# Kernel tuning notes

Hardware: AMD Instinct MI355X
Metric: run time of the kernel (lower is better)

Reference implementation:

```python
import jax, jax.numpy as jnp
import numpy as np

H = 16
D_MODEL = 1024
BLOCK_SIZE = 64
B, S = 2, 2048
NEG = -65504.0  # value used by the torch module for masking


def setup_inputs() -> dict:
    key = jax.random.key(0)
    ks = jax.random.split(key, 12)
    scale = 1.0 / np.sqrt(D_MODEL)
    inp = {
        "query": jax.random.normal(ks[0], (B, S, D_MODEL), jnp.float32),
        "key": jax.random.normal(ks[1], (B, S, D_MODEL), jnp.float32),
        "value": jax.random.normal(ks[2], (B, S, D_MODEL), jnp.float32),
        "Wq": jax.random.normal(ks[3], (D_MODEL, D_MODEL), jnp.float32) * scale,
        "bq": jnp.zeros((D_MODEL,), jnp.float32),
        "Wk": jax.random.normal(ks[4], (D_MODEL, D_MODEL), jnp.float32) * scale,
        "bk": jnp.zeros((D_MODEL,), jnp.float32),
        "Wv": jax.random.normal(ks[5], (D_MODEL, D_MODEL), jnp.float32) * scale,
        "bv": jnp.zeros((D_MODEL,), jnp.float32),
        "Wo": jax.random.normal(ks[6], (D_MODEL, D_MODEL), jnp.float32) * scale,
        "bo": jnp.zeros((D_MODEL,), jnp.float32),
    }
    return inp


def reference(query, key, value, Wq, bq, Wk, bk, Wv, bv, Wo, bo):
    b, s, d = query.shape
    dk = d // H

    def proj(x, W, bias):
        # [b,s,d] -> [b,h,s,dk]
        return (x @ W + bias).reshape(b, s, H, dk).transpose(0, 2, 1, 3)

    q = proj(query, Wq, bq)
    k = proj(key, Wk, bk)
    v = proj(value, Wv, bv)

    # dense QK^T / sqrt(d_k), exactly as the torch module (then block mask added)
    scores = jnp.einsum("bhqd,bhkd->bhqk", q, k) / jnp.sqrt(jnp.float32(dk))

    bid = jnp.arange(s) // BLOCK_SIZE
    attn_mask = jnp.where(bid[:, None] == bid[None, :], 0.0, NEG).astype(scores.dtype)
    scores = scores + attn_mask  # broadcast over [b,h]

    attn = jax.nn.softmax(scores, axis=-1)
    x = jnp.einsum("bhqk,bhkd->bhqd", attn, v)
    x = x.transpose(0, 2, 1, 3).reshape(b, s, d)
    return x @ Wo + bo
```

## Files before the change

kernel.cpp:

```cpp
#include <hip/hip_runtime.h>
#include <hip/hip_bf16.h>

typedef __attribute__((ext_vector_type(4))) float f32x4;
typedef __attribute__((ext_vector_type(8))) short s16x8;

#define MFMA16(a, b, c) __builtin_amdgcn_mfma_f32_16x16x32_bf16(a, b, c, 0, 0, 0)

__device__ __forceinline__ void gld_lds16(const void* g, void* l) {
  __builtin_amdgcn_global_load_lds(
      (const __attribute__((address_space(1))) unsigned int*)g,
      (__attribute__((address_space(3))) unsigned int*)l, 16, 0, 0);
}

__device__ __forceinline__ unsigned short f2bf(float f) {
  union { __hip_bfloat16 b; unsigned short u; } cv;
  cv.b = __float2bfloat16(f);
  return cv.u;
}
__device__ __forceinline__ float bf2f(unsigned short u) {
  union { unsigned short u; __hip_bfloat16 b; } cv;
  cv.u = u;
  return __bfloat162float(cv.b);
}

__global__ void transw(const float* W0, unsigned short* H0,
                       const float* W1, unsigned short* H1,
                       const float* W2, unsigned short* H2,
                       const float* W3, unsigned short* H3) {
  __shared__ float tile[64 * 65];
  const float* W; unsigned short* H;
  switch (blockIdx.y) {
    case 0: W = W0; H = H0; break;
    case 1: W = W1; H = H1; break;
    case 2: W = W2; H = H2; break;
    default: W = W3; H = H3; break;
  }
  const int t = threadIdx.x;
  const int tk0 = (blockIdx.x & 15) * 64;
  const int tn0 = (blockIdx.x >> 4) * 64;
  for (int i = 0; i < 16; ++i) {
    int idx = i * 256 + t;
    int r = idx >> 6, c = idx & 63;
    tile[r * 65 + c] = W[(size_t)(tk0 + r) * 1024 + tn0 + c];
  }
  __syncthreads();
  for (int i = 0; i < 16; ++i) {
    int idx = i * 256 + t;
    int r = idx >> 6, c = idx & 63;
    H[(size_t)(tn0 + r) * 1024 + tk0 + c] = f2bf(tile[c * 65 + r]);
  }
}

__global__ void convert_x3(const float* A0, unsigned short* H0,
                           const float* A1, unsigned short* H1,
                           const float* A2, unsigned short* H2) {
  const float* src; unsigned short* h;
  switch (blockIdx.y) {
    case 0: src = A0; h = H0; break;
    case 1: src = A1; h = H1; break;
    default: src = A2; h = H2; break;
  }
  int i = blockIdx.x * 256 + threadIdx.x;
  float4 v = ((const float4*)src)[i];
  ((ushort4*)h)[i] = make_ushort4(f2bf(v.x), f2bf(v.y), f2bf(v.z), f2bf(v.w));
}

struct QkvArgs {
  const unsigned short* A[3];
  const unsigned short* B[3];
  const float* bias[3];
  unsigned short* out[3];
};

__global__ __launch_bounds__(512, 2)
void gemm_qkv(QkvArgs args) {
  const int K = 1024;
  __shared__ __align__(16) unsigned short lds[4][2][8192];
  const int tid = threadIdx.x;
  const int lane = tid & 63, w = tid >> 6;

  const int nwg = 192;
  const int orig = blockIdx.x;
  const int swz = (orig & 7) * (nwg >> 3) + (orig >> 3);
  const int g = swz >> 6;
  const int tl = swz & 63;
  const int m0 = (tl >> 2) * 256, n0 = (tl & 3) * 256;

  const unsigned short* A = args.A[g];
  const unsigned short* B = args.B[g];
  const float* bias = args.bias[g];
  unsigned short* out = args.out[g];

  const int wm = (w >> 2) * 128, wn = (w & 3) * 64;
  const int fr = lane & 15, gh = lane >> 4;

  size_t aoff[2], boff[2]; int dst[2];
  #pragma unroll
  for (int i = 0; i < 2; ++i) {
    const int G = i * 512 + tid;
    const int rp = G >> 3, spr = G & 7;
    const int s = spr ^ (rp & 7);
    const int srow = 2 * rp + (s >> 2), ko = (s & 3) * 8;
    aoff[i] = (size_t)(m0 + srow) * K + ko;
    boff[i] = (size_t)(n0 + srow) * K + ko;
    dst[i] = G * 8;
  }

  auto stage = [&](int buf, int kt) {
    #pragma unroll
    for (int i = 0; i < 2; ++i) {
      gld_lds16(A + aoff[i] + kt, &lds[buf][0][dst[i]]);
      gld_lds16(B + boff[i] + kt, &lds[buf][1][dst[i]]);
    }
  };

  f32x4 acc[8][4] = {};
  const int laneoff = (fr >> 1) * 64 + ((((fr & 1) << 2) | gh) ^ (fr >> 1)) * 8;

  stage(0, 0); stage(1, 32); stage(2, 64); stage(3, 96);

  #pragma unroll 1
  for (int t = 0; t < 32; ++t) {
    if (t < 29)      { asm volatile("s_waitcnt vmcnt(12)" ::: "memory"); }
    else if (t == 29){ asm volatile("s_waitcnt vmcnt(8)"  ::: "memory"); }
    else if (t == 30){ asm volatile("s_waitcnt vmcnt(4)"  ::: "memory"); }
    else             { asm volatile("s_waitcnt vmcnt(0)"  ::: "memory"); }
    __builtin_amdgcn_s_barrier();

    const int buf = t & 3;
    const unsigned short* La = &lds[buf][0][wm * 32 + laneoff];
    const unsigned short* Lb = &lds[buf][1][wn * 32 + laneoff];
    s16x8 b[4], a[8];
    #pragma unroll
    for (int nt = 0; nt < 4; ++nt) b[nt] = *(const s16x8*)&Lb[nt * 512];
    #pragma unroll
    for (int mt = 0; mt < 8; ++mt) a[mt] = *(const s16x8*)&La[mt * 512];
    #pragma unroll
    for (int mt = 0; mt < 8; ++mt)
      #pragma unroll
      for (int nt = 0; nt < 4; ++nt)
        acc[mt][nt] = MFMA16(a[mt], b[nt], acc[mt][nt]);

    __builtin_amdgcn_sched_barrier(0);
    __builtin_amdgcn_s_barrier();
    if (t + 4 < 32) stage(buf, (t + 4) * 32);
  }

  float bv[4];
  #pragma unroll
  for (int nt = 0; nt < 4; ++nt) bv[nt] = bias[n0 + wn + nt * 16 + fr];
  if (g == 2) {
    #pragma unroll
    for (int mt = 0; mt < 8; ++mt) {
      const int gm = m0 + wm + mt * 16 + (gh << 2);
      const int b = gm >> 11, s = gm & 2047;
      #pragma unroll
      for (int nt = 0; nt < 4; ++nt) {
        const int gn = n0 + wn + nt * 16 + fr;
        const int h = gn >> 6, d = gn & 63;
        f32x4 r = acc[mt][nt];
        ushort4 w4 = make_ushort4(f2bf(r[0] + bv[nt]), f2bf(r[1] + bv[nt]),
                                  f2bf(r[2] + bv[nt]), f2bf(r[3] + bv[nt]));
        *(ushort4*)&out[((size_t)((b * 16 + h) * 64 + d)) * 2048 + s] = w4;
      }
    }
  } else {
    #pragma unroll
    for (int mt = 0; mt < 8; ++mt) {
      const int gm = m0 + wm + mt * 16 + (gh << 2);
      #pragma unroll
      for (int nt = 0; nt < 4; ++nt) {
        const int gn = n0 + wn + nt * 16 + fr;
        f32x4 r = acc[mt][nt];
        #pragma unroll
        for (int j = 0; j < 4; ++j) {
          const int row = gm + j;
          size_t off = (((size_t)((row >> 11) * 16 + (gn >> 6))) * 2048 + (row & 2047)) * 64 + (gn & 63);
          out[off] = f2bf(r[j] + bv[nt]);
        }
      }
    }
  }
}

__global__ __launch_bounds__(256, 3)
void gemm_oproj(const unsigned short* __restrict__ A, const unsigned short* __restrict__ B,
                const float* __restrict__ bias, float* __restrict__ out) {
  const int K = 1024, N = 1024;
  __shared__ __align__(16) unsigned short lds[3][2][4096];
  const int tid = threadIdx.x;
  const int lane = tid & 63, wid = tid >> 6;

  const int nwg = 256;
  const int orig = blockIdx.x;
  const int swz = (orig & 7) * (nwg >> 3) + (orig >> 3);
  const int m0 = (swz >> 3) * 128, n0 = (swz & 7) * 128;

  const int wm = (wid >> 1) * 64, wn = (wid & 1) * 64;
  const int fr = lane & 15, gh = lane >> 4;

  size_t aoff[2], boff[2]; int dst[2];
  #pragma unroll
  for (int i = 0; i < 2; ++i) {
    const int G = i * 256 + tid;
    const int rp = G >> 3, spr = G & 7;
    const int s = spr ^ (rp & 7);
    const int srow = 2 * rp + (s >> 2), ko = (s & 3) * 8;
    aoff[i] = (size_t)(m0 + srow) * K + ko;
    boff[i] = (size_t)(n0 + srow) * K + ko;
    dst[i] = G * 8;
  }

  auto stage = [&](int buf, int kt) {
    #pragma unroll
    for (int i = 0; i < 2; ++i) {
      gld_lds16(A + aoff[i] + kt, &lds[buf][0][dst[i]]);
      gld_lds16(B + boff[i] + kt, &lds[buf][1][dst[i]]);
    }
  };

  f32x4 acc[4][4] = {};
  const int laneoff = (fr >> 1) * 64 + ((((fr & 1) << 2) | gh) ^ (fr >> 1)) * 8;

  stage(0, 0); stage(1, 32); stage(2, 64);

  #pragma unroll 1
  for (int t = 0; t < 32; ++t) {
    if (t < 30)      { asm volatile("s_waitcnt vmcnt(8)" ::: "memory"); }
    else if (t == 30){ asm volatile("s_waitcnt vmcnt(4)" ::: "memory"); }
    else             { asm volatile("s_waitcnt vmcnt(0)" ::: "memory"); }
    __builtin_amdgcn_s_barrier();

    const int buf = t % 3;
    const unsigned short* La = &lds[buf][0][wm * 32 + laneoff];
    const unsigned short* Lb = &lds[buf][1][wn * 32 + laneoff];
    s16x8 b[4], a[4];
    #pragma unroll
    for (int nt = 0; nt < 4; ++nt) b[nt] = *(const s16x8*)&Lb[nt * 512];
    #pragma unroll
    for (int mt = 0; mt < 4; ++mt) a[mt] = *(const s16x8*)&La[mt * 512];
    #pragma unroll
    for (int mt = 0; mt < 4; ++mt)
      #pragma unroll
      for (int nt = 0; nt < 4; ++nt)
        acc[mt][nt] = MFMA16(a[mt], b[nt], acc[mt][nt]);

    __builtin_amdgcn_sched_barrier(0);
    __builtin_amdgcn_s_barrier();
    if (t + 3 < 32) stage(buf, (t + 3) * 32);
  }

  #pragma unroll
  for (int mt = 0; mt < 4; ++mt) {
    const int gm = m0 + wm + mt * 16 + (gh << 2);
    #pragma unroll
    for (int nt = 0; nt < 4; ++nt) {
      const int gn = n0 + wn + nt * 16 + fr;
      const float bvv = bias[gn];
      f32x4 r = acc[mt][nt];
      #pragma unroll
      for (int j = 0; j < 4; ++j)
        out[(size_t)(gm + j) * N + gn] = r[j] + bvv;
    }
  }
}

__global__ __launch_bounds__(256, 2)
void attn_mfma(const unsigned short* __restrict__ Q, const unsigned short* __restrict__ Kb,
               const unsigned short* __restrict__ Vt, unsigned short* __restrict__ X) {
  __shared__ __align__(16) unsigned short qs[4096];
  __shared__ __align__(16) unsigned short ks2[4096];
  __shared__ __align__(16) unsigned short vs[4096];
  __shared__ __align__(16) unsigned short ps[4096];
  const int tid = threadIdx.x, lane = tid & 63, w = tid >> 6;
  const int hb = blockIdx.x >> 5, qb = blockIdx.x & 31;
  const size_t qkbase = ((size_t)hb * 2048 + qb * 64) * 64;
  const size_t vbase = (size_t)hb * 64 * 2048 + qb * 64;

  #pragma unroll
  for (int i = 0; i < 2; ++i) {
    const int G = i * 256 + tid;
    const int row = G >> 3, slot = G & 7;
    const int sg = slot ^ (row & 7);
    gld_lds16(Q + qkbase + row * 64 + sg * 8, &qs[G * 8]);
    gld_lds16(Kb + qkbase + row * 64 + sg * 8, &ks2[G * 8]);
    gld_lds16(Vt + vbase + (size_t)row * 2048 + sg * 8, &vs[G * 8]);
  }
  asm volatile("s_waitcnt vmcnt(0)" ::: "memory");
  __syncthreads();

  const int fr = lane & 15, gh = lane >> 4;
  const int arow = w * 16 + fr;

  s16x8 aq[2], bk[2][4];
  #pragma unroll
  for (int ks = 0; ks < 2; ++ks) {
    aq[ks] = *(const s16x8*)&qs[arow * 64 + (((ks * 4 + gh) ^ (arow & 7)) << 3)];
    #pragma unroll
    for (int nt = 0; nt < 4; ++nt) {
      const int krow = nt * 16 + fr;
      bk[ks][nt] = *(const s16x8*)&ks2[krow * 64 + (((ks * 4 + gh) ^ (krow & 7)) << 3)];
    }
  }
  f32x4 s[4] = {};
  #pragma unroll
  for (int ks = 0; ks < 2; ++ks)
    #pragma unroll
    for (int nt = 0; nt < 4; ++nt)
      s[nt] = MFMA16(aq[ks], bk[ks][nt], s[nt]);

  #pragma unroll
  for (int j = 0; j < 4; ++j) {
    float t0 = s[0][j] * 0.125f, t1 = s[1][j] * 0.125f;
    float t2 = s[2][j] * 0.125f, t3 = s[3][j] * 0.125f;
    float m = fmaxf(fmaxf(t0, t1), fmaxf(t2, t3));
    m = fmaxf(m, __shfl_xor(m, 1, 64));
    m = fmaxf(m, __shfl_xor(m, 2, 64));
    m = fmaxf(m, __shfl_xor(m, 4, 64));
    m = fmaxf(m, __shfl_xor(m, 8, 64));
    t0 = __expf(t0 - m); t1 = __expf(t1 - m);
    t2 = __expf(t2 - m); t3 = __expf(t3 - m);
    float sum = t0 + t1 + t2 + t3;
    sum += __shfl_xor(sum, 1, 64);
    sum += __shfl_xor(sum, 2, 64);
    sum += __shfl_xor(sum, 4, 64);
    sum += __shfl_xor(sum, 8, 64);
    const float r = 1.0f / sum;
    s[0][j] = t0 * r; s[1][j] = t1 * r; s[2][j] = t2 * r; s[3][j] = t3 * r;
  }

  #pragma unroll
  for (int j = 0; j < 4; ++j) {
    const int q = w * 16 + gh * 4 + j;
    #pragma unroll
    for (int nt = 0; nt < 4; ++nt) {
      const int k = nt * 16 + fr;
      ps[q * 64 + (((k >> 3) ^ (q & 7)) << 3) + (k & 7)] = f2bf(s[nt][j]);
    }
  }

  s16x8 ap[2], bv2[2][4];
  #pragma unroll
  for (int ks = 0; ks < 2; ++ks) {
    ap[ks] = *(const s16x8*)&ps[arow * 64 + (((ks * 4 + gh) ^ (arow & 7)) << 3)];
    #pragma unroll
    for (int nt = 0; nt < 4; ++nt) {
      const int drow = nt * 16 + fr;
      bv2[ks][nt] = *(const s16x8*)&vs[drow * 64 + (((ks * 4 + gh) ^ (drow & 7)) << 3)];
    }
  }
  f32x4 x[4] = {};
  #pragma unroll
  for (int ks = 0; ks < 2; ++ks)
    #pragma unroll
    for (int nt = 0; nt < 4; ++nt)
      x[nt] = MFMA16(ap[ks], bv2[ks][nt], x[nt]);

  const int b = hb >> 4, h = hb & 15;
  #pragma unroll
  for (int nt = 0; nt < 4; ++nt)
    #pragma unroll
    for (int j = 0; j < 4; ++j) {
      const int sgl = qb * 64 + w * 16 + gh * 4 + j;
      X[((size_t)(b * 2048 + sgl)) * 1024 + h * 64 + nt * 16 + fr] = f2bf(x[nt][j]);
    }
}

extern "C" void kernel_launch(void* const* d_in, const int* in_sizes, int n_in,
                              void* d_out, int out_size, void* d_ws, size_t ws_size,
                              hipStream_t stream) {
  const float* query = (const float*)d_in[0];
  const float* key   = (const float*)d_in[1];
  const float* value = (const float*)d_in[2];
  const float* Wq = (const float*)d_in[3]; const float* bq = (const float*)d_in[4];
  const float* Wk = (const float*)d_in[5]; const float* bk = (const float*)d_in[6];
  const float* Wv = (const float*)d_in[7]; const float* bv = (const float*)d_in[8];
  const float* Wo = (const float*)d_in[9]; const float* bo = (const float*)d_in[10];
  float* out = (float*)d_out;

  const size_t W_E = 1024 * 1024;
  const size_t X_E = 4096 * 1024;
  unsigned char* p = (unsigned char*)d_ws;
  auto take = [&](size_t bytes) { void* r = (void*)p; p += bytes; return r; };

  unsigned short* wtq = (unsigned short*)take(W_E * 2);
  unsigned short* wtk = (unsigned short*)take(W_E * 2);
  unsigned short* wtv = (unsigned short*)take(W_E * 2);
  unsigned short* wto = (unsigned short*)take(W_E * 2);
  unsigned short* xq = (unsigned short*)take(X_E * 2);
  unsigned short* xk = (unsigned short*)take(X_E * 2);
  unsigned short* xv = (unsigned short*)take(X_E * 2);
  unsigned short* Qb = (unsigned short*)take(X_E * 2);
  unsigned short* Kb = (unsigned short*)take(X_E * 2);
  unsigned short* Vt = (unsigned short*)take(X_E * 2);
  unsigned short* ao = (unsigned short*)take(X_E * 2);
  (void)ws_size; (void)in_sizes; (void)n_in; (void)out_size;

  transw<<<dim3(256, 4), 256, 0, stream>>>(Wq, wtq, Wk, wtk, Wv, wtv, Wo, wto);
  convert_x3<<<dim3(4096, 3), 256, 0, stream>>>(query, xq, key, xk, value, xv);

  QkvArgs qkv = {};
  qkv.A[0] = xq; qkv.B[0] = wtq; qkv.bias[0] = bq; qkv.out[0] = Qb;
  qkv.A[1] = xk; qkv.B[1] = wtk; qkv.bias[1] = bk; qkv.out[1] = Kb;
  qkv.A[2] = xv; qkv.B[2] = wtv; qkv.bias[2] = bv; qkv.out[2] = Vt;
  gemm_qkv<<<dim3(192), 512, 0, stream>>>(qkv);

  attn_mfma<<<dim3(1024), 256, 0, stream>>>(Qb, Kb, Vt, ao);

  gemm_oproj<<<dim3(256), 256, 0, stream>>>(ao, wto, bo, out);
}
```

Measured before the change: 86.72 us.

## Restructure GEMM main loops into ping-pong phases with interleaved loads and setprio

Both projection GEMM kernels now issue the next global-to-LDS stage inside the iteration, overlapped with the MFMA work, instead of after it. The QKV GEMM splits each k-step into two halves, loading A then B for a stage three steps ahead, with barriers between halves and s_setprio raised around the MFMA blocks. The output GEMM keeps a prefetch distance of two instead of three and moves its vmcnt wait to the end of the iteration. The intent is to hide LDS reads and global load issue behind matrix math and reduce stalls at barriers. In exchange there are more barriers per iteration, and the reuse of LDS buffers needs exact waitcnt bookkeeping to avoid races.

```diff
diff --git a/kernel.cpp b/kernel.cpp
--- a/kernel.cpp
+++ b/kernel.cpp
@@ -106,44 +106,68 @@
     dst[i] = G * 8;
   }
 
-  auto stage = [&](int buf, int kt) {
-    #pragma unroll
-    for (int i = 0; i < 2; ++i) {
-      gld_lds16(A + aoff[i] + kt, &lds[buf][0][dst[i]]);
-      gld_lds16(B + boff[i] + kt, &lds[buf][1][dst[i]]);
-    }
+  auto stageA = [&](int buf, int kt) {
+    gld_lds16(A + aoff[0] + kt, &lds[buf][0][dst[0]]);
+    gld_lds16(A + aoff[1] + kt, &lds[buf][0][dst[1]]);
+  };
+  auto stageB = [&](int buf, int kt) {
+    gld_lds16(B + boff[0] + kt, &lds[buf][1][dst[0]]);
+    gld_lds16(B + boff[1] + kt, &lds[buf][1][dst[1]]);
   };
 
   f32x4 acc[8][4] = {};
   const int laneoff = (fr >> 1) * 64 + ((((fr & 1) << 2) | gh) ^ (fr >> 1)) * 8;
 
-  stage(0, 0); stage(1, 32); stage(2, 64); stage(3, 96);
+  stageA(0, 0);  stageB(0, 0);
+  stageA(1, 32); stageB(1, 32);
+  stageA(2, 64); stageB(2, 64);
+  asm volatile("s_waitcnt vmcnt(8)" ::: "memory");
+  __builtin_amdgcn_s_barrier();
+  __builtin_amdgcn_sched_barrier(0);
 
   #pragma unroll 1
   for (int t = 0; t < 32; ++t) {
-    if (t < 29)      { asm volatile("s_waitcnt vmcnt(12)" ::: "memory"); }
-    else if (t == 29){ asm volatile("s_waitcnt vmcnt(8)"  ::: "memory"); }
-    else if (t == 30){ asm volatile("s_waitcnt vmcnt(4)"  ::: "memory"); }
-    else             { asm volatile("s_waitcnt vmcnt(0)"  ::: "memory"); }
-    __builtin_amdgcn_s_barrier();
-
     const int buf = t & 3;
     const unsigned short* La = &lds[buf][0][wm * 32 + laneoff];
     const unsigned short* Lb = &lds[buf][1][wn * 32 + laneoff];
-    s16x8 b[4], a[8];
+    s16x8 a[8], b[4];
+
     #pragma unroll
     for (int nt = 0; nt < 4; ++nt) b[nt] = *(const s16x8*)&Lb[nt * 512];
     #pragma unroll
-    for (int mt = 0; mt < 8; ++mt) a[mt] = *(const s16x8*)&La[mt * 512];
-    #pragma unroll
-    for (int mt = 0; mt < 8; ++mt)
+    for (int mt = 0; mt < 4; ++mt) a[mt] = *(const s16x8*)&La[mt * 512];
+    if (t <= 28) stageA((t + 3) & 3, (t + 3) * 32);
+    __builtin_amdgcn_s_barrier();
+    asm volatile("s_waitcnt lgkmcnt(0)" ::: "memory");
+    __builtin_amdgcn_sched_barrier(0);
+    __builtin_amdgcn_s_setprio(1);
+    #pragma unroll
+    for (int mt = 0; mt < 4; ++mt)
       #pragma unroll
       for (int nt = 0; nt < 4; ++nt)
         acc[mt][nt] = MFMA16(a[mt], b[nt], acc[mt][nt]);
-
-    __builtin_amdgcn_sched_barrier(0);
-    __builtin_amdgcn_s_barrier();
-    if (t + 4 < 32) stage(buf, (t + 4) * 32);
+    __builtin_amdgcn_s_setprio(0);
+    __builtin_amdgcn_s_barrier();
+    __builtin_amdgcn_sched_barrier(0);
+
+    #pragma unroll
+    for (int mt = 4; mt < 8; ++mt) a[mt] = *(const s16x8*)&La[mt * 512];
+    if (t <= 28) stageB((t + 3) & 3, (t + 3) * 32);
+    __builtin_amdgcn_s_barrier();
+    asm volatile("s_waitcnt lgkmcnt(0)" ::: "memory");
+    __builtin_amdgcn_sched_barrier(0);
+    __builtin_amdgcn_s_setprio(1);
+    #pragma unroll
+    for (int mt = 4; mt < 8; ++mt)
+      #pragma unroll
+      for (int nt = 0; nt < 4; ++nt)
+        acc[mt][nt] = MFMA16(a[mt], b[nt], acc[mt][nt]);
+    __builtin_amdgcn_s_setprio(0);
+    if (t < 29)       { asm volatile("s_waitcnt vmcnt(8)" ::: "memory"); }
+    else if (t == 29) { asm volatile("s_waitcnt vmcnt(4)" ::: "memory"); }
+    else if (t == 30) { asm volatile("s_waitcnt vmcnt(0)" ::: "memory"); }
+    __builtin_amdgcn_s_barrier();
+    __builtin_amdgcn_sched_barrier(0);
   }
 
   float bv[4];
@@ -153,7 +177,7 @@
     #pragma unroll
     for (int mt = 0; mt < 8; ++mt) {
       const int gm = m0 + wm + mt * 16 + (gh << 2);
-      const int b = gm >> 11, s = gm & 2047;
+      const int b2 = gm >> 11, s = gm & 2047;
       #pragma unroll
       for (int nt = 0; nt < 4; ++nt) {
         const int gn = n0 + wn + nt * 16 + fr;
@@ -161,7 +185,7 @@
         f32x4 r = acc[mt][nt];
         ushort4 w4 = make_ushort4(f2bf(r[0] + bv[nt]), f2bf(r[1] + bv[nt]),
                                   f2bf(r[2] + bv[nt]), f2bf(r[3] + bv[nt]));
-        *(ushort4*)&out[((size_t)((b * 16 + h) * 64 + d)) * 2048 + s] = w4;
+        *(ushort4*)&out[((size_t)((b2 * 16 + h) * 64 + d)) * 2048 + s] = w4;
       }
     }
   } else {
@@ -222,15 +246,13 @@
   f32x4 acc[4][4] = {};
   const int laneoff = (fr >> 1) * 64 + ((((fr & 1) << 2) | gh) ^ (fr >> 1)) * 8;
 
-  stage(0, 0); stage(1, 32); stage(2, 64);
+  stage(0, 0); stage(1, 32);
+  asm volatile("s_waitcnt vmcnt(4)" ::: "memory");
+  __builtin_amdgcn_s_barrier();
+  __builtin_amdgcn_sched_barrier(0);
 
   #pragma unroll 1
   for (int t = 0; t < 32; ++t) {
-    if (t < 30)      { asm volatile("s_waitcnt vmcnt(8)" ::: "memory"); }
-    else if (t == 30){ asm volatile("s_waitcnt vmcnt(4)" ::: "memory"); }
-    else             { asm volatile("s_waitcnt vmcnt(0)" ::: "memory"); }
-    __builtin_amdgcn_s_barrier();
-
     const int buf = t % 3;
     const unsigned short* La = &lds[buf][0][wm * 32 + laneoff];
     const unsigned short* Lb = &lds[buf][1][wn * 32 + laneoff];
@@ -239,15 +261,21 @@
     for (int nt = 0; nt < 4; ++nt) b[nt] = *(const s16x8*)&Lb[nt * 512];
     #pragma unroll
     for (int mt = 0; mt < 4; ++mt) a[mt] = *(const s16x8*)&La[mt * 512];
+    if (t <= 29) stage((t + 2) % 3, (t + 2) * 32);
+    __builtin_amdgcn_s_barrier();
+    asm volatile("s_waitcnt lgkmcnt(0)" ::: "memory");
+    __builtin_amdgcn_sched_barrier(0);
+    __builtin_amdgcn_s_setprio(1);
     #pragma unroll
     for (int mt = 0; mt < 4; ++mt)
       #pragma unroll
       for (int nt = 0; nt < 4; ++nt)
         acc[mt][nt] = MFMA16(a[mt], b[nt], acc[mt][nt]);
-
-    __builtin_amdgcn_sched_barrier(0);
-    __builtin_amdgcn_s_barrier();
-    if (t + 3 < 32) stage(buf, (t + 3) * 32);
+    __builtin_amdgcn_s_setprio(0);
+    if (t < 30)       { asm volatile("s_waitcnt vmcnt(4)" ::: "memory"); }
+    else if (t == 30) { asm volatile("s_waitcnt vmcnt(0)" ::: "memory"); }
+    __builtin_amdgcn_s_barrier();
+    __builtin_amdgcn_sched_barrier(0);
   }
 
   #pragma unroll
```

Result: no change. 85.48 us (-1.4%).
